# Optimization experiments

Measured on AMD Instinct MI355X. Metric: run time of the kernel, lower is better.

Reference implementation:

```python
import jax, jax.numpy as jnp
import numpy as np

NUM_RELS = 64
EDGES_PER_REL = 16384
N_NODES = 100000
IN_FEAT = 128
OUT_FEAT = 128
NUM_BASES = 16
E = NUM_RELS * EDGES_PER_REL


def setup_inputs() -> dict:
    key = jax.random.key(0)
    ks = jax.random.split(key, 8)
    feat = jax.random.normal(ks[0], (N_NODES, IN_FEAT), dtype=jnp.float32)
    weight = jax.random.normal(ks[1], (NUM_BASES, IN_FEAT, OUT_FEAT), dtype=jnp.float32) * 0.05
    w_comp = jax.random.normal(ks[2], (NUM_RELS, NUM_BASES), dtype=jnp.float32) * 0.3
    h_bias = jnp.zeros((OUT_FEAT,), dtype=jnp.float32)
    loop_weight = jax.random.normal(ks[3], (IN_FEAT, OUT_FEAT), dtype=jnp.float32) * 0.05
    norm = jax.random.uniform(ks[4], (E, 1), dtype=jnp.float32)
    src = jax.random.randint(ks[5], (E,), 0, N_NODES, dtype=jnp.int32).astype(jnp.int64)
    dst = jax.random.randint(ks[6], (E,), 0, N_NODES, dtype=jnp.int32).astype(jnp.int64)
    # edges are sorted by relation type with uniform per-relation sections
    etypes = jnp.repeat(jnp.arange(NUM_RELS, dtype=jnp.int64), EDGES_PER_REL)
    return {"feat": feat, "weight": weight, "w_comp": w_comp, "h_bias": h_bias,
            "loop_weight": loop_weight, "norm": norm, "src": src, "dst": dst,
            "etypes": etypes, "section": EDGES_PER_REL}


def reference(feat, weight, w_comp, h_bias, loop_weight, norm, src, dst, etypes, section):
    num_rels, num_bases = w_comp.shape
    n_nodes, in_feat = feat.shape
    out_feat = weight.shape[2]
    # basis composition: per-relation weights [R, in, out]
    W = jnp.matmul(w_comp, weight.reshape(num_bases, in_feat * out_feat))
    W = W.reshape(num_rels, in_feat, out_feat)
    # gather per-edge source features (edges sorted by relation, uniform sections)
    h_e = feat[src]                                   # [E, in]
    n_edges = h_e.shape[0]
    h_r = h_e.reshape(num_rels, section, in_feat)     # [R, e_r, in]
    msg = jnp.einsum('rei,rio->reo', h_r, W)          # grouped matmul
    msg = msg.reshape(n_edges, out_feat) * norm       # edge-norm scaling
    # scatter-sum aggregation to destination nodes
    node_repr = jax.ops.segment_sum(msg, dst, num_segments=n_nodes)
    node_repr = node_repr + h_bias + jnp.matmul(feat, loop_weight)
    return jax.nn.relu(node_repr)
```

## Files before the change

### kernel.cpp

```cpp
#include <hip/hip_runtime.h>

#define N_NODES 100000
#define N_PAD 100352
#define NBLK 392
#define IN_FEAT 128
#define OUT_FEAT 128
#define NUM_RELS 64
#define EDGES_PER_REL 16384
#define NUM_BASES 16
#define E_TOTAL (NUM_RELS * EDGES_PER_REL)

typedef __bf16 bf16x8 __attribute__((ext_vector_type(8)));
typedef float floatx4 __attribute__((ext_vector_type(4)));

__global__ __launch_bounds__(256) void feat_to_bf16_kernel(
    const float* __restrict__ feat, __bf16* __restrict__ fb) {
  long i = ((long)blockIdx.x * 256 + threadIdx.x) * 8;
  float4 a = *(const float4*)(feat + i);
  float4 b = *(const float4*)(feat + i + 4);
  __bf16 t8[8] = {(__bf16)a.x, (__bf16)a.y, (__bf16)a.z, (__bf16)a.w,
                  (__bf16)b.x, (__bf16)b.y, (__bf16)b.z, (__bf16)b.w};
  *(uint4*)(fb + i) = *(uint4*)t8;
}

__global__ __launch_bounds__(256) void compose_w_bf16_kernel(
    const float* __restrict__ weight, const float* __restrict__ w_comp,
    __bf16* __restrict__ Wp) {
  int idx = blockIdx.x * 256 + threadIdx.x;
  int r = idx >> 14;
  int off = idx & 16383;
  int j = off & 7, n = (off >> 3) & 127, kp = off >> 10;
  int k = kp * 8 + j;
  const float* wc = w_comp + r * NUM_BASES;
  float acc = 0.f;
#pragma unroll
  for (int b = 0; b < NUM_BASES; ++b)
    acc += wc[b] * weight[b * 16384 + k * 128 + n];
  Wp[idx] = (__bf16)acc;
}

__global__ __launch_bounds__(256) void pack_loop_w_kernel(
    const float* __restrict__ loop_w, __bf16* __restrict__ Lp) {
  int idx = blockIdx.x * 256 + threadIdx.x;
  int j = idx & 7, n = (idx >> 3) & 127, kp = idx >> 10;
  Lp[idx] = (__bf16)loop_w[(kp * 8 + j) * 128 + n];
}

__global__ __launch_bounds__(256) void compose_w_f32_kernel(
    const float* __restrict__ weight, const float* __restrict__ w_comp,
    float* __restrict__ W) {
  int idx = blockIdx.x * 256 + threadIdx.x;
  int r = idx >> 14;
  int io = idx & 16383;
  const float* wc = w_comp + r * NUM_BASES;
  float acc = 0.f;
#pragma unroll
  for (int b = 0; b < NUM_BASES; ++b)
    acc += wc[b] * weight[b * 16384 + io];
  W[idx] = acc;
}

__global__ __launch_bounds__(256) void init_out_mfma(
    const float* __restrict__ feat, const __bf16* __restrict__ featb,
    const __bf16* __restrict__ Lp, const float* __restrict__ bias,
    float* __restrict__ out) {
  __shared__ __bf16 A_lds[64 * 136];
  int t = threadIdx.x;
  long base = (long)blockIdx.x * 64;
  if (featb) {
#pragma unroll
    for (int j = 0; j < 4; ++j) {
      int idx = t + j * 256;
      int e = idx >> 4, seg = idx & 15;
      long n = base + e;
      uint4 v = make_uint4(0u, 0u, 0u, 0u);
      if (n < N_NODES) v = ((const uint4*)featb)[n * 16 + seg];
      *(uint4*)&A_lds[e * 136 + seg * 8] = v;
    }
  } else {
#pragma unroll
    for (int j = 0; j < 8; ++j) {
      int idx = t + j * 256;
      int e = idx >> 5, k4 = idx & 31;
      long n = base + e;
      float4 v = make_float4(0.f, 0.f, 0.f, 0.f);
      if (n < N_NODES) v = ((const float4*)feat)[n * 32 + k4];
      __bf16 tb[4] = {(__bf16)v.x, (__bf16)v.y, (__bf16)v.z, (__bf16)v.w};
      *(ushort4*)&A_lds[e * 136 + k4 * 4] = *(ushort4*)tb;
    }
  }
  __syncthreads();

  int wave = t >> 6, lane = t & 63;
  int m16 = lane & 15, quad = lane >> 4;
  floatx4 acc[8];
#pragma unroll
  for (int nt = 0; nt < 8; ++nt) acc[nt] = (floatx4){0.f, 0.f, 0.f, 0.f};

  const __bf16* a_base = &A_lds[(wave * 16 + m16) * 136 + quad * 8];
#pragma unroll
  for (int ks = 0; ks < 4; ++ks) {
    bf16x8 a = *(const bf16x8*)(a_base + ks * 32);
    int kp = ks * 4 + quad;
#pragma unroll
    for (int nt = 0; nt < 8; ++nt) {
      bf16x8 b = *(const bf16x8*)(Lp + (kp * 128 + nt * 16 + m16) * 8);
      acc[nt] = __builtin_amdgcn_mfma_f32_16x16x32_bf16(a, b, acc[nt], 0, 0, 0);
    }
  }

  float bv[8];
#pragma unroll
  for (int nt = 0; nt < 8; ++nt) bv[nt] = bias[nt * 16 + m16];
#pragma unroll
  for (int r = 0; r < 4; ++r) {
    long n = base + wave * 16 + quad * 4 + r;
    if (n < N_NODES) {
#pragma unroll
      for (int nt = 0; nt < 8; ++nt)
        out[n * 128 + nt * 16 + m16] = acc[nt][r] + bv[nt];
    }
  }
}

__global__ __launch_bounds__(256) void zero_kernel(int* __restrict__ p) {
  p[blockIdx.x * 256 + threadIdx.x] = 0;
}

__global__ __launch_bounds__(256) void hist8_kernel(
    const int* __restrict__ dst, int* __restrict__ cnt8, int cshift) {
  int e = blockIdx.x * 256 + threadIdx.x;
  int c = e >> cshift;
  atomicAdd(&cnt8[c * N_PAD + dst[e]], 1);
}

__global__ __launch_bounds__(256) void scan1_kernel(
    const int* __restrict__ cnt, int* __restrict__ row,
    int* __restrict__ bsum) {
  __shared__ int s[256];
  int t = threadIdx.x;
  int idx = blockIdx.x * 256 + t;
  int v = cnt[idx];
  s[t] = v;
  __syncthreads();
  for (int o = 1; o < 256; o <<= 1) {
    int x = (t >= o) ? s[t - o] : 0;
    __syncthreads();
    s[t] += x;
    __syncthreads();
  }
  row[idx] = s[t] - v;
  if (t == 255) bsum[blockIdx.x] = s[t];
}

__global__ __launch_bounds__(512) void scan2_kernel(
    const int* __restrict__ bsum, int* __restrict__ boff) {
  __shared__ int s[512];
  int t = threadIdx.x;
  int v = (t < NBLK) ? bsum[blockIdx.x * NBLK + t] : 0;
  s[t] = v;
  __syncthreads();
  for (int o = 1; o < 512; o <<= 1) {
    int x = (t >= o) ? s[t - o] : 0;
    __syncthreads();
    s[t] += x;
    __syncthreads();
  }
  if (t < NBLK) boff[blockIdx.x * NBLK + t] = s[t] - v;
}

__global__ __launch_bounds__(256) void scan3_kernel(
    int* __restrict__ row, const int* __restrict__ boff,
    int* __restrict__ fill) {
  int idx = blockIdx.x * 256 + threadIdx.x;
  int v = row[idx] + boff[blockIdx.x];
  row[idx] = v;
  fill[idx] = v;
}

__global__ __launch_bounds__(256) void scatter_pos_kernel(
    const int* __restrict__ dst, int* __restrict__ fill8,
    int* __restrict__ pos, int cshift) {
  int e = blockIdx.x * 256 + threadIdx.x;
  int c = e >> cshift;
  pos[e] = atomicAdd(&fill8[c * N_PAD + dst[e]], 1);
}

__global__ __launch_bounds__(256) void edge_gemm_mfma(
    const float* __restrict__ feat, const __bf16* __restrict__ featb,
    const __bf16* __restrict__ Wp, const float* __restrict__ norm,
    const int* __restrict__ src, const int* __restrict__ pos,
    unsigned short* __restrict__ msg, int e_lo) {
  __shared__ __bf16 A_lds[64 * 136];
  __shared__ int s_src[64];
  __shared__ int s_pos[64];
  __shared__ float s_norm[64];
  int t = threadIdx.x;
  long base = (long)e_lo + (long)blockIdx.x * 64;
  int rel = (int)(base >> 14);
  const __bf16* Wr = Wp + (long)rel * (IN_FEAT * OUT_FEAT);

  if (t < 64) {
    s_src[t] = src[base + t];
    s_pos[t] = pos[base + t];
    s_norm[t] = norm[base + t];
  }
  __syncthreads();
  if (featb) {
#pragma unroll
    for (int j = 0; j < 4; ++j) {
      int idx = t + j * 256;
      int e = idx >> 4, seg = idx & 15;
      uint4 v = ((const uint4*)featb)[(long)s_src[e] * 16 + seg];
      *(uint4*)&A_lds[e * 136 + seg * 8] = v;
    }
  } else {
#pragma unroll
    for (int j = 0; j < 8; ++j) {
      int idx = t + j * 256;
      int e = idx >> 5, k4 = idx & 31;
      float4 v = ((const float4*)feat)[(long)s_src[e] * 32 + k4];
      __bf16 tb[4] = {(__bf16)v.x, (__bf16)v.y, (__bf16)v.z, (__bf16)v.w};
      *(ushort4*)&A_lds[e * 136 + k4 * 4] = *(ushort4*)tb;
    }
  }
  __syncthreads();

  int wave = t >> 6, lane = t & 63;
  int m16 = lane & 15, quad = lane >> 4;
  floatx4 acc[8];
#pragma unroll
  for (int nt = 0; nt < 8; ++nt) acc[nt] = (floatx4){0.f, 0.f, 0.f, 0.f};

  const __bf16* a_base = &A_lds[(wave * 16 + m16) * 136 + quad * 8];
#pragma unroll
  for (int ks = 0; ks < 4; ++ks) {
    bf16x8 a = *(const bf16x8*)(a_base + ks * 32);
    int kp = ks * 4 + quad;
#pragma unroll
    for (int nt = 0; nt < 8; ++nt) {
      bf16x8 b = *(const bf16x8*)(Wr + (kp * 128 + nt * 16 + m16) * 8);
      acc[nt] = __builtin_amdgcn_mfma_f32_16x16x32_bf16(a, b, acc[nt], 0, 0, 0);
    }
  }

  __syncthreads();
#pragma unroll
  for (int r = 0; r < 4; ++r) {
    int erow = wave * 16 + quad * 4 + r;
    float nm = s_norm[erow];
#pragma unroll
    for (int nt = 0; nt < 8; ++nt)
      A_lds[erow * 136 + nt * 16 + m16] = (__bf16)(acc[nt][r] * nm);
  }
  __syncthreads();
#pragma unroll
  for (int it = 0; it < 4; ++it) {
    int idx = it * 256 + t;
    int row = idx >> 4, seg = idx & 15;
    uint4 v = *(const uint4*)&A_lds[row * 136 + seg * 8];
    *(uint4*)(msg + (long)s_pos[row] * 128 + seg * 8) = v;
  }
}

__global__ __launch_bounds__(256) void gather_csr_kernel(
    const unsigned short* __restrict__ msg, const int* __restrict__ rowc,
    float* __restrict__ out, int do_relu) {
  int wave = threadIdx.x >> 6, lane = threadIdx.x & 63;
  int n = blockIdx.x * 4 + wave;
  if (n >= N_NODES) return;
  int beg = rowc[n], end = rowc[n + 1];
  if (!do_relu && beg == end) return;
  int half = lane >> 5;
  int c4 = lane & 31;
  float s0 = 0.f, s1 = 0.f, s2 = 0.f, s3 = 0.f;
  for (int j = beg + half; j < end; j += 2) {
    uint2 m = *(const uint2*)(msg + (long)j * 128 + c4 * 4);
    s0 += __uint_as_float(m.x << 16);
    s1 += __uint_as_float(m.x & 0xFFFF0000u);
    s2 += __uint_as_float(m.y << 16);
    s3 += __uint_as_float(m.y & 0xFFFF0000u);
  }
  s0 += __shfl_down(s0, 32);
  s1 += __shfl_down(s1, 32);
  s2 += __shfl_down(s2, 32);
  s3 += __shfl_down(s3, 32);
  if (half == 0) {
    float4 o = ((float4*)out)[(long)n * 32 + c4];
    o.x += s0; o.y += s1; o.z += s2; o.w += s3;
    if (do_relu) {
      o.x = fmaxf(o.x, 0.f); o.y = fmaxf(o.y, 0.f);
      o.z = fmaxf(o.z, 0.f); o.w = fmaxf(o.w, 0.f);
    }
    ((float4*)out)[(long)n * 32 + c4] = o;
  }
}

__global__ __launch_bounds__(256) void init_out_f32_kernel(
    const float* __restrict__ feat, const float* __restrict__ loop_w,
    const float* __restrict__ bias, float* __restrict__ out) {
  __shared__ float4 A4[64][32];
  int t = threadIdx.x;
  long base = (long)blockIdx.x * 64;
#pragma unroll
  for (int j = 0; j < 8; ++j) {
    int idx = t + j * 256;
    int e = idx >> 5, k4 = idx & 31;
    long n = base + e;
    float4 v = make_float4(0.f, 0.f, 0.f, 0.f);
    if (n < N_NODES) v = ((const float4*)feat)[n * 32 + k4];
    A4[e][k4] = v;
  }
  __syncthreads();
  int og = t & 31, eg = t >> 5;
  float acc[8][4];
#pragma unroll
  for (int j = 0; j < 8; ++j)
#pragma unroll
    for (int d = 0; d < 4; ++d) acc[j][d] = 0.f;
  const float4* W4 = (const float4*)loop_w;
  for (int k4 = 0; k4 < 32; ++k4) {
    float4 a[8];
#pragma unroll
    for (int j = 0; j < 8; ++j) a[j] = A4[eg * 8 + j][k4];
#pragma unroll
    for (int d = 0; d < 4; ++d) {
      float4 w = W4[(k4 * 4 + d) * 32 + og];
#pragma unroll
      for (int j = 0; j < 8; ++j) {
        float av = ((const float*)&a[j])[d];
        acc[j][0] += av * w.x;
        acc[j][1] += av * w.y;
        acc[j][2] += av * w.z;
        acc[j][3] += av * w.w;
      }
    }
  }
  float4 b = ((const float4*)bias)[og];
#pragma unroll
  for (int j = 0; j < 8; ++j) {
    long n = base + eg * 8 + j;
    if (n < N_NODES) {
      float4 v = make_float4(acc[j][0] + b.x, acc[j][1] + b.y,
                             acc[j][2] + b.z, acc[j][3] + b.w);
      ((float4*)out)[n * 32 + og] = v;
    }
  }
}

__global__ __launch_bounds__(256) void edge_msg_atomic_kernel(
    const float* __restrict__ feat, const float* __restrict__ W,
    const float* __restrict__ norm, const int* __restrict__ src,
    const int* __restrict__ dst, float* __restrict__ out) {
  __shared__ float4 A4[64][32];
  __shared__ int s_src[64];
  __shared__ int s_dst[64];
  __shared__ float s_norm[64];
  int t = threadIdx.x;
  long base = (long)blockIdx.x * 64;
  int rel = blockIdx.x >> 8;
  const float4* Wr4 = (const float4*)(W + (long)rel * IN_FEAT * OUT_FEAT);
  if (t < 64) {
    s_src[t] = src[base + t];
    s_dst[t] = dst[base + t];
    s_norm[t] = norm[base + t];
  }
  __syncthreads();
#pragma unroll
  for (int j = 0; j < 8; ++j) {
    int idx = t + j * 256;
    int e = idx >> 5, k4 = idx & 31;
    A4[e][k4] = ((const float4*)feat)[(long)s_src[e] * 32 + k4];
  }
  __syncthreads();
  int og = t & 31, eg = t >> 5;
  float acc[8][4];
#pragma unroll
  for (int j = 0; j < 8; ++j)
#pragma unroll
    for (int d = 0; d < 4; ++d) acc[j][d] = 0.f;
  for (int k4 = 0; k4 < 32; ++k4) {
    float4 a[8];
#pragma unroll
    for (int j = 0; j < 8; ++j) a[j] = A4[eg * 8 + j][k4];
#pragma unroll
    for (int d = 0; d < 4; ++d) {
      float4 w = Wr4[(k4 * 4 + d) * 32 + og];
#pragma unroll
      for (int j = 0; j < 8; ++j) {
        float av = ((const float*)&a[j])[d];
        acc[j][0] += av * w.x;
        acc[j][1] += av * w.y;
        acc[j][2] += av * w.z;
        acc[j][3] += av * w.w;
      }
    }
  }
#pragma unroll
  for (int j = 0; j < 8; ++j) {
    int e = eg * 8 + j;
    float nm = s_norm[e];
    float* orow = out + (long)s_dst[e] * OUT_FEAT + og * 4;
#pragma unroll
    for (int d = 0; d < 4; ++d) atomicAdd(orow + d, acc[j][d] * nm);
  }
}

__global__ __launch_bounds__(256) void relu_kernel(float* __restrict__ out) {
  int idx = blockIdx.x * 256 + threadIdx.x;
  float4 v = ((const float4*)out)[idx];
  v.x = fmaxf(v.x, 0.f);
  v.y = fmaxf(v.y, 0.f);
  v.z = fmaxf(v.z, 0.f);
  v.w = fmaxf(v.w, 0.f);
  ((float4*)out)[idx] = v;
}

extern "C" void kernel_launch(void* const* d_in, const int* in_sizes, int n_in,
                              void* d_out, int out_size, void* d_ws, size_t ws_size,
                              hipStream_t stream) {
  const float* feat   = (const float*)d_in[0];
  const float* weight = (const float*)d_in[1];
  const float* w_comp = (const float*)d_in[2];
  const float* h_bias = (const float*)d_in[3];
  const float* loop_w = (const float*)d_in[4];
  const float* norm   = (const float*)d_in[5];
  const int*   src    = (const int*)d_in[6];
  const int*   dst    = (const int*)d_in[7];
  float* out = (float*)d_out;

  const size_t SZ_WP  = (size_t)NUM_RELS * IN_FEAT * OUT_FEAT * 2;
  const size_t SZ_LP  = (size_t)IN_FEAT * OUT_FEAT * 2;
  const size_t SZ_FB  = (size_t)N_NODES * IN_FEAT * 2;
  const size_t SZ_POS = (size_t)E_TOTAL * 4;

  int CH = 0, FB = 0;
  {
    const int chs[10] = {64, 32, 32, 16, 16, 8, 8, 4, 4, 0};
    const int fbs[10] = { 1,  1,  0,  1,  0, 1, 0, 1, 0, 0};
    for (int i = 0; i < 9 && CH == 0; ++i) {
      int ch = chs[i], fb = fbs[i], nc = NUM_RELS / ch;
      size_t need = SZ_WP + SZ_LP + (fb ? SZ_FB : 0) + SZ_POS +
                    2 * (size_t)nc * N_PAD * 4 + 2 * (size_t)nc * NBLK * 4 +
                    (size_t)ch * EDGES_PER_REL * OUT_FEAT * 2;
      if (ws_size >= need) { CH = ch; FB = fb; }
    }
  }

  if (CH > 0) {
    const int NC = NUM_RELS / CH;
    const int chunk_edges = CH * EDGES_PER_REL;
    int cshift = 14;
    for (int x = CH; x > 1; x >>= 1) ++cshift;

    char* p = (char*)d_ws;
    __bf16* Wp = (__bf16*)p;                  p += SZ_WP;
    __bf16* Lp = (__bf16*)p;                  p += SZ_LP;
    __bf16* featb = nullptr;
    if (FB) { featb = (__bf16*)p;             p += SZ_FB; }
    int* pos  = (int*)p;                      p += SZ_POS;
    int* cnt8 = (int*)p;                      p += (size_t)NC * N_PAD * 4;
    int* row8 = (int*)p;                      p += (size_t)NC * N_PAD * 4;
    int* bsum = (int*)p;                      p += (size_t)NC * NBLK * 4;
    int* boff = (int*)p;                      p += (size_t)NC * NBLK * 4;
    unsigned short* msg = (unsigned short*)p;

    if (FB)
      hipLaunchKernelGGL(feat_to_bf16_kernel,
                         dim3(N_NODES * IN_FEAT / 8 / 256), dim3(256), 0,
                         stream, feat, featb);
    hipLaunchKernelGGL(pack_loop_w_kernel, dim3(16384 / 256), dim3(256), 0,
                       stream, loop_w, Lp);
    hipLaunchKernelGGL(init_out_mfma, dim3((N_NODES + 63) / 64), dim3(256), 0,
                       stream, feat, featb, Lp, h_bias, out);
    hipLaunchKernelGGL(compose_w_bf16_kernel, dim3(NUM_RELS * 16384 / 256),
                       dim3(256), 0, stream, weight, w_comp, Wp);
    hipLaunchKernelGGL(zero_kernel, dim3(NC * NBLK), dim3(256), 0, stream, cnt8);
    hipLaunchKernelGGL(hist8_kernel, dim3(E_TOTAL / 256), dim3(256), 0, stream,
                       dst, cnt8, cshift);
    hipLaunchKernelGGL(scan1_kernel, dim3(NC * NBLK), dim3(256), 0, stream,
                       cnt8, row8, bsum);
    hipLaunchKernelGGL(scan2_kernel, dim3(NC), dim3(512), 0, stream, bsum, boff);
    hipLaunchKernelGGL(scan3_kernel, dim3(NC * NBLK), dim3(256), 0, stream,
                       row8, boff, cnt8);
    hipLaunchKernelGGL(scatter_pos_kernel, dim3(E_TOTAL / 256), dim3(256), 0,
                       stream, dst, cnt8, pos, cshift);

    for (int c = 0; c < NC; ++c) {
      hipLaunchKernelGGL(edge_gemm_mfma, dim3(chunk_edges / 64), dim3(256), 0,
                         stream, feat, featb, Wp, norm, src, pos, msg,
                         c * chunk_edges);
      hipLaunchKernelGGL(gather_csr_kernel, dim3((N_NODES + 3) / 4), dim3(256),
                         0, stream, msg, row8 + (size_t)c * N_PAD, out,
                         (c == NC - 1) ? 1 : 0);
    }
  } else {
    float* W = (float*)d_ws;
    hipLaunchKernelGGL(init_out_f32_kernel, dim3((N_NODES + 63) / 64),
                       dim3(256), 0, stream, feat, loop_w, h_bias, out);
    hipLaunchKernelGGL(compose_w_f32_kernel, dim3(NUM_RELS * 16384 / 256),
                       dim3(256), 0, stream, weight, w_comp, W);
    hipLaunchKernelGGL(edge_msg_atomic_kernel, dim3(E_TOTAL / 64), dim3(256), 0,
                       stream, feat, W, norm, src, dst, out);
    hipLaunchKernelGGL(relu_kernel, dim3((N_NODES * OUT_FEAT / 4) / 256),
                       dim3(256), 0, stream, out);
  }
}
```

Baseline: 446.1 us.

## Fuse weight packing kernels, emit bf16 features from init, stage W in LDS

Merges the relation-weight composition and loop-weight packing into one launch. The separate feat-to-bf16 pass is removed: init_out_mfma now writes the bf16 copy of the features while it converts them for its own GEMM. edge_gemm_mfma copies the relation's 32 KB packed weight tile into LDS and reads MFMA B operands from there instead of global memory. This saves two launches and one full pass over the features. In exchange it raises LDS use per block to about 50 KB, which may reduce occupancy, and adds a 32 KB global-to-LDS copy per 64-edge block.

```diff
diff --git a/kernel.cpp b/kernel.cpp
--- a/kernel.cpp
+++ b/kernel.cpp
@@ -13,37 +13,27 @@
 typedef __bf16 bf16x8 __attribute__((ext_vector_type(8)));
 typedef float floatx4 __attribute__((ext_vector_type(4)));
 
-__global__ __launch_bounds__(256) void feat_to_bf16_kernel(
-    const float* __restrict__ feat, __bf16* __restrict__ fb) {
-  long i = ((long)blockIdx.x * 256 + threadIdx.x) * 8;
-  float4 a = *(const float4*)(feat + i);
-  float4 b = *(const float4*)(feat + i + 4);
-  __bf16 t8[8] = {(__bf16)a.x, (__bf16)a.y, (__bf16)a.z, (__bf16)a.w,
-                  (__bf16)b.x, (__bf16)b.y, (__bf16)b.z, (__bf16)b.w};
-  *(uint4*)(fb + i) = *(uint4*)t8;
-}
-
-__global__ __launch_bounds__(256) void compose_w_bf16_kernel(
+__global__ __launch_bounds__(256) void compose_all_bf16_kernel(
     const float* __restrict__ weight, const float* __restrict__ w_comp,
-    __bf16* __restrict__ Wp) {
-  int idx = blockIdx.x * 256 + threadIdx.x;
-  int r = idx >> 14;
-  int off = idx & 16383;
-  int j = off & 7, n = (off >> 3) & 127, kp = off >> 10;
-  int k = kp * 8 + j;
-  const float* wc = w_comp + r * NUM_BASES;
-  float acc = 0.f;
-#pragma unroll
-  for (int b = 0; b < NUM_BASES; ++b)
-    acc += wc[b] * weight[b * 16384 + k * 128 + n];
-  Wp[idx] = (__bf16)acc;
-}
-
-__global__ __launch_bounds__(256) void pack_loop_w_kernel(
-    const float* __restrict__ loop_w, __bf16* __restrict__ Lp) {
-  int idx = blockIdx.x * 256 + threadIdx.x;
-  int j = idx & 7, n = (idx >> 3) & 127, kp = idx >> 10;
-  Lp[idx] = (__bf16)loop_w[(kp * 8 + j) * 128 + n];
+    const float* __restrict__ loop_w, __bf16* __restrict__ Wp,
+    __bf16* __restrict__ Lp) {
+  int gid = blockIdx.x * 256 + threadIdx.x;
+  if (gid < NUM_RELS * 16384) {
+    int r = gid >> 14;
+    int off = gid & 16383;
+    int j = off & 7, n = (off >> 3) & 127, kp = off >> 10;
+    int k = kp * 8 + j;
+    const float* wc = w_comp + r * NUM_BASES;
+    float acc = 0.f;
+#pragma unroll
+    for (int b = 0; b < NUM_BASES; ++b)
+      acc += wc[b] * weight[b * 16384 + k * 128 + n];
+    Wp[gid] = (__bf16)acc;
+  } else {
+    int idx = gid - NUM_RELS * 16384;
+    int j = idx & 7, n = (idx >> 3) & 127, kp = idx >> 10;
+    Lp[idx] = (__bf16)loop_w[(kp * 8 + j) * 128 + n];
+  }
 }
 
 __global__ __launch_bounds__(256) void compose_w_f32_kernel(
@@ -61,33 +51,24 @@
 }
 
 __global__ __launch_bounds__(256) void init_out_mfma(
-    const float* __restrict__ feat, const __bf16* __restrict__ featb,
+    const float* __restrict__ feat, __bf16* __restrict__ featb,
     const __bf16* __restrict__ Lp, const float* __restrict__ bias,
     float* __restrict__ out) {
   __shared__ __bf16 A_lds[64 * 136];
   int t = threadIdx.x;
   long base = (long)blockIdx.x * 64;
-  if (featb) {
-#pragma unroll
-    for (int j = 0; j < 4; ++j) {
-      int idx = t + j * 256;
-      int e = idx >> 4, seg = idx & 15;
-      long n = base + e;
-      uint4 v = make_uint4(0u, 0u, 0u, 0u);
-      if (n < N_NODES) v = ((const uint4*)featb)[n * 16 + seg];
-      *(uint4*)&A_lds[e * 136 + seg * 8] = v;
-    }
-  } else {
-#pragma unroll
-    for (int j = 0; j < 8; ++j) {
-      int idx = t + j * 256;
-      int e = idx >> 5, k4 = idx & 31;
-      long n = base + e;
-      float4 v = make_float4(0.f, 0.f, 0.f, 0.f);
-      if (n < N_NODES) v = ((const float4*)feat)[n * 32 + k4];
-      __bf16 tb[4] = {(__bf16)v.x, (__bf16)v.y, (__bf16)v.z, (__bf16)v.w};
-      *(ushort4*)&A_lds[e * 136 + k4 * 4] = *(ushort4*)tb;
-    }
+#pragma unroll
+  for (int j = 0; j < 8; ++j) {
+    int idx = t + j * 256;
+    int e = idx >> 5, k4 = idx & 31;
+    long n = base + e;
+    float4 v = make_float4(0.f, 0.f, 0.f, 0.f);
+    bool ok = (n < N_NODES);
+    if (ok) v = ((const float4*)feat)[n * 32 + k4];
+    __bf16 tb[4] = {(__bf16)v.x, (__bf16)v.y, (__bf16)v.z, (__bf16)v.w};
+    *(ushort4*)&A_lds[e * 136 + k4 * 4] = *(ushort4*)tb;
+    if (featb && ok)
+      *(ushort4*)(featb + n * 128 + k4 * 4) = *(ushort4*)tb;
   }
   __syncthreads();
 
@@ -192,6 +173,7 @@
     const int* __restrict__ src, const int* __restrict__ pos,
     unsigned short* __restrict__ msg, int e_lo) {
   __shared__ __bf16 A_lds[64 * 136];
+  __shared__ __bf16 B_lds[IN_FEAT * OUT_FEAT];
   __shared__ int s_src[64];
   __shared__ int s_pos[64];
   __shared__ float s_norm[64];
@@ -204,6 +186,12 @@
     s_src[t] = src[base + t];
     s_pos[t] = pos[base + t];
     s_norm[t] = norm[base + t];
+  }
+  {
+    const uint4* Wr4 = (const uint4*)Wr;
+    uint4* B4 = (uint4*)B_lds;
+#pragma unroll
+    for (int j = 0; j < 8; ++j) B4[t + j * 256] = Wr4[t + j * 256];
   }
   __syncthreads();
   if (featb) {
@@ -239,7 +227,7 @@
     int kp = ks * 4 + quad;
 #pragma unroll
     for (int nt = 0; nt < 8; ++nt) {
-      bf16x8 b = *(const bf16x8*)(Wr + (kp * 128 + nt * 16 + m16) * 8);
+      bf16x8 b = *(const bf16x8*)(B_lds + (kp * 128 + nt * 16 + m16) * 8);
       acc[nt] = __builtin_amdgcn_mfma_f32_16x16x32_bf16(a, b, acc[nt], 0, 0, 0);
     }
   }
@@ -465,16 +453,11 @@
     int* boff = (int*)p;                      p += (size_t)NC * NBLK * 4;
     unsigned short* msg = (unsigned short*)p;
 
-    if (FB)
-      hipLaunchKernelGGL(feat_to_bf16_kernel,
-                         dim3(N_NODES * IN_FEAT / 8 / 256), dim3(256), 0,
-                         stream, feat, featb);
-    hipLaunchKernelGGL(pack_loop_w_kernel, dim3(16384 / 256), dim3(256), 0,
-                       stream, loop_w, Lp);
+    hipLaunchKernelGGL(compose_all_bf16_kernel,
+                       dim3((NUM_RELS * 16384 + 16384) / 256), dim3(256), 0,
+                       stream, weight, w_comp, loop_w, Wp, Lp);
     hipLaunchKernelGGL(init_out_mfma, dim3((N_NODES + 63) / 64), dim3(256), 0,
                        stream, feat, featb, Lp, h_bias, out);
-    hipLaunchKernelGGL(compose_w_bf16_kernel, dim3(NUM_RELS * 16384 / 256),
-                       dim3(256), 0, stream, weight, w_comp, Wp);
     hipLaunchKernelGGL(zero_kernel, dim3(NC * NBLK), dim3(256), 0, stream, cnt8);
     hipLaunchKernelGGL(hist8_kernel, dim3(E_TOTAL / 256), dim3(256), 0, stream,
                        dst, cnt8, cshift);
```

New measurement: 432.1 us. 1.03x faster.
